# Optimization experiments

Hardware: AMD Instinct MI355X
Metric: run time of the kernel (lower is better)

The kernel has to match this reference:

```python
import jax, jax.numpy as jnp
import numpy as np

N_HEADS = 12
HEAD_DIM = 32
H_OUT = 28
W_OUT = 28
EPS_LN = 1e-6
EPS_TS = 1e-6


def _layer_norm(x, g, eps=EPS_LN):
    mu = jnp.mean(x, axis=-1, keepdims=True)
    xc = x - mu
    var = jnp.mean(xc * xc, axis=-1, keepdims=True)
    return xc * jax.lax.rsqrt(var + eps) * g


def setup_inputs() -> dict:
    key = jax.random.key(0)
    ks = jax.random.split(key, 6)
    b, hh, ww, d = 4, 56, 56, 384
    nc = 2 * H_OUT * W_OUT  # 1568
    s = 0.02
    return {
        "x": jax.random.normal(ks[0], (b, hh, ww, d), jnp.float32),
        "clusters": jax.random.normal(ks[1], (b, nc, d), jnp.float32),
        "g1": jnp.ones((d,), jnp.float32),
        "Wq": jax.random.normal(ks[2], (d, d), jnp.float32) * s,
        "Wkv": jax.random.normal(ks[3], (d, 2 * d), jnp.float32) * s,
        "Wo": jax.random.normal(ks[4], (d, d), jnp.float32) * s,
        "res_scale": jnp.ones((d,), jnp.float32),
        "g2": jnp.ones((2 * d,), jnp.float32),
        "Wproj": jax.random.normal(ks[5], (2 * d, 768), jnp.float32) * s,
    }


def reference(x, clusters, g1, Wq, Wkv, Wo, res_scale, g2, Wproj):
    b, hh, ww, d = x.shape
    n = hh * ww
    nc = clusters.shape[1]
    dh = HEAD_DIM
    scale = dh ** -0.5

    xf = x.reshape(b, n, d)
    xn = _layer_norm(xf, g1)
    cn = _layer_norm(clusters, g1)

    # projections; rearrange 'b n (h d) -> b h n d' and 'b n (k h d) -> k b h n d'
    q = (cn @ Wq).reshape(b, nc, N_HEADS, dh).transpose(0, 2, 1, 3)
    kv = (xn @ Wkv).reshape(b, n, 2, N_HEADS, dh)
    k = kv[:, :, 0].transpose(0, 2, 1, 3)  # [b h n dh]
    v = kv[:, :, 1].transpose(0, 2, 1, 3)

    attn = jnp.einsum('bhqd,bhkd->bhqk', q, k) * scale  # [b h nc n]
    # soft assignment: softmax over the query (cluster) axis
    attn = jax.nn.softmax(attn, axis=-2)
    token_sizes = attn.sum(-1)  # [b h nc]
    attn = attn / (token_sizes[..., None] + EPS_TS)
    token_sizes = token_sizes.mean(1)  # [b nc]

    c2 = jnp.einsum('bhqk,bhkd->bhqd', attn, v)
    c2 = c2.transpose(0, 2, 1, 3).reshape(b, nc, d) @ Wo

    token_sizes = token_sizes.reshape(b, nc // 2, 2).sum(-1)  # [b n']

    y = clusters * res_scale + c2
    y = y.reshape(b, nc // 2, 2 * d)  # 'b (n two) d -> b n (two d)'
    y = _layer_norm(y, g2) @ Wproj
    y = y.reshape(b, H_OUT, W_OUT, -1)
    token_sizes = token_sizes.reshape(b, H_OUT, W_OUT)
    return y, token_sizes
```

## Files before the change

kernel.cpp:

```cpp
#include <hip/hip_runtime.h>
#include <hip/hip_bf16.h>

typedef __hip_bfloat16 bf16;
typedef __attribute__((ext_vector_type(8))) short short8;
typedef __attribute__((ext_vector_type(4))) float f32x4;

#define B 4
#define NT 3136
#define NC 1568
#define NP 784
#define DMODEL 384
#define D2 768
#define NH 12
#define DH 32
#define KSPLIT 2
#define KSPLIT0 1600
#define SCALE 0.17677669529663687f
#define LOG2E 1.4426950408889634f
#define EPS_LN 1e-6f
#define EPS_TS 1e-6f

#if __has_builtin(__builtin_amdgcn_exp2f)
#define EXP2(x) __builtin_amdgcn_exp2f(x)
#else
#define EXP2(x) __expf(0.6931471805599453f * (x))
#endif

__device__ __forceinline__ unsigned short f2bf(float f) {
  return (unsigned short)(__bfloat16_as_ushort(__float2bfloat16(f)));
}
__device__ __forceinline__ float b2f(unsigned short u) {
  return __uint_as_float(((unsigned int)u) << 16);
}

__device__ __forceinline__ float lda(const void* __restrict__ p, size_t i,
                                     int mode, bool inf32) {
  bool f32 = (mode == 2) || (mode == 1 && inf32);
  return f32 ? ((const float*)p)[i]
             : __bfloat162float(((const bf16*)p)[i]);
}
__device__ __forceinline__ float4 lda4(const void* __restrict__ p, size_t i,
                                       int mode, bool inf32) {
  bool f32 = (mode == 2) || (mode == 1 && inf32);
  if (f32) return *(const float4*)((const float*)p + i);
  ushort4 u = *(const ushort4*)((const bf16*)p + i);
  return make_float4(b2f(u.x), b2f(u.y), b2f(u.z), b2f(u.w));
}

__global__ void sniff_kernel(const unsigned short* __restrict__ g1,
                             int* __restrict__ flag) {
  if (threadIdx.x == 0 && blockIdx.x == 0)
    *flag = (g1[0] == 0x3F80) ? 0 : 1;
}

__global__ void transpose_kernel(const void* __restrict__ in,
                                 const int* __restrict__ dtf,
                                 bf16* __restrict__ out, int K, int N,
                                 float scale) {
  bool inf32 = (*dtf != 0);
  __shared__ float t[32][33];
  int n0 = blockIdx.x * 32, k0 = blockIdx.y * 32;
  int tx = threadIdx.x & 31, ty = threadIdx.x >> 5;
#pragma unroll
  for (int s = 0; s < 32; s += 8)
    t[ty + s][tx] = lda(in, (size_t)(k0 + ty + s) * N + n0 + tx, 1, inf32);
  __syncthreads();
#pragma unroll
  for (int s = 0; s < 32; s += 8)
    out[(size_t)(n0 + ty + s) * K + k0 + tx] =
        __float2bfloat16(t[tx][ty + s] * scale);
}

__global__ void stats_kernel(const void* __restrict__ in, int mode,
                             const int* __restrict__ dtf,
                             float* __restrict__ stats, int D) {
  bool inf32 = (*dtf != 0);
  int row = blockIdx.x;
  int tid = threadIdx.x;
  size_t base = (size_t)row * D;
  int nper = D >> 7;
  float s = 0.f, s2 = 0.f;
  for (int i = 0; i < nper; i++) {
    float xv = lda(in, base + tid + (i << 7), mode, inf32);
    s += xv; s2 += xv * xv;
  }
  __shared__ float red[128], red2[128];
  red[tid] = s; red2[tid] = s2;
  __syncthreads();
  for (int off = 64; off > 0; off >>= 1) {
    if (tid < off) { red[tid] += red[tid + off]; red2[tid] += red2[tid + off]; }
    __syncthreads();
  }
  if (tid == 0) {
    float mean = red[0] / (float)D;
    float var  = red2[0] / (float)D - mean * mean;
    stats[row * 2]     = mean;
    stats[row * 2 + 1] = rsqrtf(var + EPS_LN);
  }
}

__global__ void __launch_bounds__(256, 3)
mgemm_kernel(const void* __restrict__ A, int a_mode, size_t a_bstr,
             const float* __restrict__ Astats, size_t s_bstr,
             const void* __restrict__ gammaA,
             const bf16* __restrict__ BT,
             const int* __restrict__ dtf,
             void* __restrict__ C, int c_f32, size_t c_bstr,
             bf16* __restrict__ Cv,
             int M, int N, int K,
             int epi,
             const void* __restrict__ resid, size_t r_bstr,
             const void* __restrict__ rscale) {
  bool inf32 = (*dtf != 0);
  int z = blockIdx.z;
  size_t a_off = (size_t)z * a_bstr;
  size_t r_off = (size_t)z * r_bstr;
  const float* st = Astats ? Astats + (size_t)z * s_bstr : nullptr;
  __shared__ __align__(16) unsigned short Asl[128][40];
  __shared__ __align__(16) unsigned short Bsl[128][40];
  int tid = threadIdx.x;
  int wave = tid >> 6, lane = tid & 63, l16 = lane & 15, quad = lane >> 4;
  int brow = blockIdx.y * 128, bcol = blockIdx.x * 128;
  int wm = (wave >> 1) * 64, wn = (wave & 1) * 64;
  f32x4 acc[4][4];
#pragma unroll
  for (int i = 0; i < 4; i++)
#pragma unroll
    for (int j = 0; j < 4; j++) acc[i][j] = (f32x4){0.f, 0.f, 0.f, 0.f};

  for (int k0 = 0; k0 < K; k0 += 32) {
#pragma unroll
    for (int it = 0; it < 4; it++) {
      int i = it * 256 + tid;
      int r = i >> 3, c4 = (i & 7) * 4;
      int grow = brow + r;
      if (grow >= M) grow = M - 1;
      float4 v = lda4(A, a_off + (size_t)grow * K + k0 + c4, a_mode, inf32);
      if (st) {
        float mu = st[grow * 2], rstd = st[grow * 2 + 1];
        float4 g = lda4(gammaA, k0 + c4, 1, inf32);
        v.x = (v.x - mu) * rstd * g.x; v.y = (v.y - mu) * rstd * g.y;
        v.z = (v.z - mu) * rstd * g.z; v.w = (v.w - mu) * rstd * g.w;
      }
      ushort4 u = {f2bf(v.x), f2bf(v.y), f2bf(v.z), f2bf(v.w)};
      *(ushort4*)&Asl[r][c4] = u;
    }
#pragma unroll
    for (int it = 0; it < 4; it++) {
      int i = it * 256 + tid;
      int r = i >> 3, c4 = (i & 7) * 4;
      *(ushort4*)&Bsl[r][c4] =
          *(const ushort4*)(BT + (size_t)(bcol + r) * K + k0 + c4);
    }
    __syncthreads();
    short8 af[4], bfr[4];
#pragma unroll
    for (int i = 0; i < 4; i++)
      af[i] = *(const short8*)&Asl[wm + 16 * i + l16][quad * 8];
#pragma unroll
    for (int j = 0; j < 4; j++)
      bfr[j] = *(const short8*)&Bsl[wn + 16 * j + l16][quad * 8];
#pragma unroll
    for (int i = 0; i < 4; i++)
#pragma unroll
      for (int j = 0; j < 4; j++)
        acc[i][j] = __builtin_amdgcn_mfma_f32_16x16x32_bf16(
            af[i], bfr[j], acc[i][j], 0, 0, 0);
    __syncthreads();
  }
#pragma unroll
  for (int i = 0; i < 4; i++) {
#pragma unroll
    for (int r = 0; r < 4; r++) {
      int m = brow + wm + 16 * i + quad * 4 + r;
      if (m < M) {
#pragma unroll
        for (int j = 0; j < 4; j++) {
          int n = bcol + wn + 16 * j + l16;
          float v = acc[i][j][r];
          if (epi == 1)
            v += lda(resid, r_off + (size_t)m * N + n, 1, inf32) *
                 lda(rscale, n, 1, inf32);
          if (epi == 2) {
            if (n < DMODEL) {
              ((bf16*)C)[(size_t)z * c_bstr + (size_t)m * DMODEL + n] =
                  __float2bfloat16(v);
            } else {
              int cc = n - DMODEL, hh = cc >> 5, dd = cc & 31;
              int w = m & 31;
              int pos = ((w >> 2) & 3) * 8 + (w >> 4) * 4 + (w & 3);
              Cv[(((size_t)z * NH + hh) * DH + dd) * NT + (m & ~31) + pos] =
                  __float2bfloat16(v);
            }
          } else {
            size_t idx = (size_t)z * c_bstr + (size_t)m * N + n;
            if (c_f32) ((float*)C)[idx] = v;
            else       ((bf16*)C)[idx]  = __float2bfloat16(v);
          }
        }
      }
    }
  }
}

__global__ void __launch_bounds__(256, 4)
sgemm_kernel(const void* __restrict__ A, int a_mode, size_t a_bstr,
             const float* __restrict__ Astats, size_t s_bstr,
             const void* __restrict__ gammaA,
             const bf16* __restrict__ BT,
             const int* __restrict__ dtf,
             void* __restrict__ C, int c_f32, size_t c_bstr,
             int M, int N, int K, int epi,
             const void* __restrict__ resid, size_t r_bstr,
             const void* __restrict__ rscale) {
  bool inf32 = (*dtf != 0);
  int z = blockIdx.z;
  size_t a_off = (size_t)z * a_bstr;
  size_t r_off = (size_t)z * r_bstr;
  const float* st = Astats ? Astats + (size_t)z * s_bstr : nullptr;
  int tid = threadIdx.x;
  int wave = tid >> 6, lane = tid & 63, l16 = lane & 15, quad = lane >> 4;
  int n0 = (blockIdx.x * 4 + wave) * 32;
  int m0 = blockIdx.y * 32;
  int ra = m0 + l16, rb = m0 + 16 + l16;
  int rca = (ra < M) ? ra : M - 1;
  int rcb = (rb < M) ? rb : M - 1;
  float mua = 0.f, rsa = 1.f, mub = 0.f, rsb = 1.f;
  if (st) {
    mua = st[rca * 2]; rsa = st[rca * 2 + 1];
    mub = st[rcb * 2]; rsb = st[rcb * 2 + 1];
  }
  const bf16* b0p = BT + (size_t)(n0 + l16) * K;
  const bf16* b1p = BT + (size_t)(n0 + 16 + l16) * K;
  f32x4 acc00 = {0.f, 0.f, 0.f, 0.f}, acc01 = {0.f, 0.f, 0.f, 0.f};
  f32x4 acc10 = {0.f, 0.f, 0.f, 0.f}, acc11 = {0.f, 0.f, 0.f, 0.f};
  for (int k0 = 0; k0 < K; k0 += 32) {
    int ka = k0 + quad * 8;
    float4 v0 = lda4(A, a_off + (size_t)rca * K + ka,     a_mode, inf32);
    float4 v1 = lda4(A, a_off + (size_t)rca * K + ka + 4, a_mode, inf32);
    float4 w0 = lda4(A, a_off + (size_t)rcb * K + ka,     a_mode, inf32);
    float4 w1 = lda4(A, a_off + (size_t)rcb * K + ka + 4, a_mode, inf32);
    if (st) {
      float4 g0  = lda4(gammaA, ka,     1, inf32);
      float4 g1v = lda4(gammaA, ka + 4, 1, inf32);
      v0.x = (v0.x - mua) * rsa * g0.x;  v0.y = (v0.y - mua) * rsa * g0.y;
      v0.z = (v0.z - mua) * rsa * g0.z;  v0.w = (v0.w - mua) * rsa * g0.w;
      v1.x = (v1.x - mua) * rsa * g1v.x; v1.y = (v1.y - mua) * rsa * g1v.y;
      v1.z = (v1.z - mua) * rsa * g1v.z; v1.w = (v1.w - mua) * rsa * g1v.w;
      w0.x = (w0.x - mub) * rsb * g0.x;  w0.y = (w0.y - mub) * rsb * g0.y;
      w0.z = (w0.z - mub) * rsb * g0.z;  w0.w = (w0.w - mub) * rsb * g0.w;
      w1.x = (w1.x - mub) * rsb * g1v.x; w1.y = (w1.y - mub) * rsb * g1v.y;
      w1.z = (w1.z - mub) * rsb * g1v.z; w1.w = (w1.w - mub) * rsb * g1v.w;
    }
    short8 afa, afb;
    afa[0] = (short)f2bf(v0.x); afa[1] = (short)f2bf(v0.y);
    afa[2] = (short)f2bf(v0.z); afa[3] = (short)f2bf(v0.w);
    afa[4] = (short)f2bf(v1.x); afa[5] = (short)f2bf(v1.y);
    afa[6] = (short)f2bf(v1.z); afa[7] = (short)f2bf(v1.w);
    afb[0] = (short)f2bf(w0.x); afb[1] = (short)f2bf(w0.y);
    afb[2] = (short)f2bf(w0.z); afb[3] = (short)f2bf(w0.w);
    afb[4] = (short)f2bf(w1.x); afb[5] = (short)f2bf(w1.y);
    afb[6] = (short)f2bf(w1.z); afb[7] = (short)f2bf(w1.w);
    short8 bf0 = *(const short8*)(b0p + ka);
    short8 bf1 = *(const short8*)(b1p + ka);
    acc00 = __builtin_amdgcn_mfma_f32_16x16x32_bf16(afa, bf0, acc00, 0, 0, 0);
    acc01 = __builtin_amdgcn_mfma_f32_16x16x32_bf16(afa, bf1, acc01, 0, 0, 0);
    acc10 = __builtin_amdgcn_mfma_f32_16x16x32_bf16(afb, bf0, acc10, 0, 0, 0);
    acc11 = __builtin_amdgcn_mfma_f32_16x16x32_bf16(afb, bf1, acc11, 0, 0, 0);
  }
#pragma unroll
  for (int i = 0; i < 2; i++) {
#pragma unroll
    for (int r = 0; r < 4; r++) {
      int m = m0 + 16 * i + quad * 4 + r;
      if (m >= M) continue;
      float v0 = (i == 0) ? acc00[r] : acc10[r];
      float v1 = (i == 0) ? acc01[r] : acc11[r];
      int nA = n0 + l16, nB = n0 + 16 + l16;
      if (epi == 1) {
        v0 += lda(resid, r_off + (size_t)m * N + nA, 1, inf32) *
              lda(rscale, nA, 1, inf32);
        v1 += lda(resid, r_off + (size_t)m * N + nB, 1, inf32) *
              lda(rscale, nB, 1, inf32);
      }
      size_t i0 = (size_t)z * c_bstr + (size_t)m * N + nA;
      size_t i1 = (size_t)z * c_bstr + (size_t)m * N + nB;
      if (c_f32) {
        ((float*)C)[i0] = v0;
        ((float*)C)[i1] = v1;
      } else {
        ((bf16*)C)[i0] = __float2bfloat16(v0);
        ((bf16*)C)[i1] = __float2bfloat16(v1);
      }
    }
  }
}

__global__ void __launch_bounds__(256, 4)
colsum_mfma(const bf16* __restrict__ qm, const bf16* __restrict__ km,
            float* __restrict__ l2ci) {
  int b = blockIdx.z, h = blockIdx.y;
  int tid = threadIdx.x;
  int wave = tid >> 6, lane = tid & 63, l16 = lane & 15, quad = lane >> 4;
  int key0 = blockIdx.x * 128 + wave * 32 + l16;
  int key1 = key0 + 16;
  int kc0 = (key0 < NT) ? key0 : NT - 1;
  int kc1 = (key1 < NT) ? key1 : NT - 1;
  short8 kf0 = *(const short8*)(km +
      ((size_t)(b * NT + kc0) * DMODEL + h * DH + quad * 8));
  short8 kf1 = *(const short8*)(km +
      ((size_t)(b * NT + kc1) * DMODEL + h * DH + quad * 8));
  __shared__ __align__(16) unsigned short Qlds[32][40];
  const bf16* qb = qm + (size_t)b * NC * DMODEL + h * DH;
  int srow = tid >> 3, sc4 = (tid & 7) * 4;
  float cs0 = 0.f, cs1 = 0.f;
  for (int q0 = 0; q0 < NC; q0 += 32) {
    ushort4 qu = *(const ushort4*)(qb + (size_t)(q0 + srow) * DMODEL + sc4);
    __syncthreads();
    *(ushort4*)&Qlds[srow][sc4] = qu;
    __syncthreads();
    short8 a1 = *(const short8*)&Qlds[l16][quad * 8];
    short8 a2 = *(const short8*)&Qlds[16 + l16][quad * 8];
    f32x4 z = {0.f, 0.f, 0.f, 0.f};
    f32x4 s10 = __builtin_amdgcn_mfma_f32_16x16x32_bf16(a1, kf0, z, 0, 0, 0);
    f32x4 s20 = __builtin_amdgcn_mfma_f32_16x16x32_bf16(a2, kf0, z, 0, 0, 0);
    f32x4 s11 = __builtin_amdgcn_mfma_f32_16x16x32_bf16(a1, kf1, z, 0, 0, 0);
    f32x4 s21 = __builtin_amdgcn_mfma_f32_16x16x32_bf16(a2, kf1, z, 0, 0, 0);
#pragma unroll
    for (int r = 0; r < 4; r++) {
      cs0 += EXP2(s10[r]) + EXP2(s20[r]);
      cs1 += EXP2(s11[r]) + EXP2(s21[r]);
    }
  }
  cs0 += __shfl_xor(cs0, 16, 64);
  cs0 += __shfl_xor(cs0, 32, 64);
  cs1 += __shfl_xor(cs1, 16, 64);
  cs1 += __shfl_xor(cs1, 32, 64);
  if (quad == 0) {
    if (key0 < NT) l2ci[((size_t)b * NH + h) * NT + key0] = -__log2f(cs0);
    if (key1 < NT) l2ci[((size_t)b * NH + h) * NT + key1] = -__log2f(cs1);
  }
}

__global__ void __launch_bounds__(256, 4)
pv_mfma(const bf16* __restrict__ qm, const bf16* __restrict__ km,
        const bf16* __restrict__ vt, const float* __restrict__ l2ci,
        float* __restrict__ po, float* __restrict__ prs) {
  int z = blockIdx.z;
  int b = z >> 1, split = z & 1;
  int h = blockIdx.y;
  int tid = threadIdx.x;
  int wave = tid >> 6, lane = tid & 63, l16 = lane & 15, quad = lane >> 4;
  int q0w = blockIdx.x * 128 + wave * 32;
  short8 qfrag[2];
#pragma unroll
  for (int t = 0; t < 2; t++) {
    int qr = q0w + t * 16 + l16; if (qr >= NC) qr = NC - 1;
    qfrag[t] = *(const short8*)(qm +
        ((size_t)(b * NC + qr) * DMODEL + h * DH + quad * 8));
  }
  __shared__ __align__(16) unsigned short Klds[64][40];
  __shared__ __align__(16) unsigned short Vlds[32][72];
  __shared__ __align__(16) float csl[64];
  f32x4 olo[2], ohi[2];
#pragma unroll
  for (int t = 0; t < 2; t++) {
    olo[t] = (f32x4){0.f, 0.f, 0.f, 0.f};
    ohi[t] = (f32x4){0.f, 0.f, 0.f, 0.f};
  }
  float rs[2] = {0.f, 0.f};
  const float* csb = l2ci + ((size_t)b * NH + h) * NT;
  const bf16* kb = km + (size_t)b * NT * DMODEL + h * DH;
  const bf16* vtb = vt + ((size_t)b * NH + h) * DH * NT;
  int krow = tid >> 2, kc8 = (tid & 3) * 8;
  int vrow = tid >> 3, vc8 = (tid & 7) * 8;
  int kbeg = split ? KSPLIT0 : 0;
  int kend = split ? NT : KSPLIT0;
  for (int k0 = kbeg; k0 < kend; k0 += 64) {
    short8 ku = *(const short8*)(kb + (size_t)(k0 + krow) * DMODEL + kc8);
    short8 vu = *(const short8*)(vtb + (size_t)vrow * NT + k0 + vc8);
    float4 cf;
    if (tid < 16) cf = *(const float4*)(csb + k0 + tid * 4);
    __syncthreads();
    *(short8*)&Klds[krow][kc8] = ku;
    *(short8*)&Vlds[vrow][vc8] = vu;
    if (tid < 16) *(float4*)&csl[tid * 4] = cf;
    __syncthreads();
#pragma unroll
    for (int ks = 0; ks < 64; ks += 32) {
      short8 kf1 = *(const short8*)&Klds[ks + l16][quad * 8];
      short8 kf2 = *(const short8*)&Klds[ks + 16 + l16][quad * 8];
      float4 ci1 = *(const float4*)&csl[ks + quad * 4];
      float4 ci2 = *(const float4*)&csl[ks + 16 + quad * 4];
      short8 vlo = *(const short8*)&Vlds[l16][ks + quad * 8];
      short8 vhi = *(const short8*)&Vlds[16 + l16][ks + quad * 8];
#pragma unroll
      for (int t = 0; t < 2; t++) {
        f32x4 z4 = {0.f, 0.f, 0.f, 0.f};
        f32x4 s1 = __builtin_amdgcn_mfma_f32_16x16x32_bf16(kf1, qfrag[t], z4, 0, 0, 0);
        f32x4 s2 = __builtin_amdgcn_mfma_f32_16x16x32_bf16(kf2, qfrag[t], z4, 0, 0, 0);
        float p0 = EXP2(s1[0] + ci1.x);
        float p1 = EXP2(s1[1] + ci1.y);
        float p2 = EXP2(s1[2] + ci1.z);
        float p3 = EXP2(s1[3] + ci1.w);
        float p4 = EXP2(s2[0] + ci2.x);
        float p5 = EXP2(s2[1] + ci2.y);
        float p6 = EXP2(s2[2] + ci2.z);
        float p7 = EXP2(s2[3] + ci2.w);
        rs[t] += ((p0 + p1) + (p2 + p3)) + ((p4 + p5) + (p6 + p7));
        short8 pf;
        pf[0] = (short)f2bf(p0); pf[1] = (short)f2bf(p1);
        pf[2] = (short)f2bf(p2); pf[3] = (short)f2bf(p3);
        pf[4] = (short)f2bf(p4); pf[5] = (short)f2bf(p5);
        pf[6] = (short)f2bf(p6); pf[7] = (short)f2bf(p7);
        olo[t] = __builtin_amdgcn_mfma_f32_16x16x32_bf16(pf, vlo, olo[t], 0, 0, 0);
        ohi[t] = __builtin_amdgcn_mfma_f32_16x16x32_bf16(pf, vhi, ohi[t], 0, 0, 0);
      }
    }
  }
#pragma unroll
  for (int t = 0; t < 2; t++) {
    rs[t] += __shfl_xor(rs[t], 16, 64);
    rs[t] += __shfl_xor(rs[t], 32, 64);
  }
  size_t pb = ((size_t)(split * B + b) * NH + h) * NC;
#pragma unroll
  for (int t = 0; t < 2; t++) {
#pragma unroll
    for (int r = 0; r < 4; r++) {
      int qloc = quad * 4 + r;
      int q = q0w + t * 16 + qloc;
      if (q < NC) {
        po[(pb + q) * 32 + l16]      = olo[t][r];
        po[(pb + q) * 32 + 16 + l16] = ohi[t][r];
      }
    }
    int qr = q0w + t * 16 + l16;
    if (quad == 0 && qr < NC) prs[pb + qr] = rs[t];
  }
}

__global__ void combine_kernel(const float* __restrict__ po,
                               const float* __restrict__ prs,
                               bf16* __restrict__ c2) {
  int bh = blockIdx.y;
  int tid = threadIdx.x;
  int q = blockIdx.x * 8 + (tid >> 5);
  int d = tid & 31;
  int b = bh / NH, h = bh - b * NH;
  size_t base0 = (size_t)bh * NC;
  size_t base1 = (size_t)B * NH * NC + base0;
  float o = po[(base0 + q) * 32 + d] + po[(base1 + q) * 32 + d];
  float rs = prs[base0 + q] + prs[base1 + q];
  c2[((size_t)b * NC + q) * DMODEL + h * 32 + d] =
      __float2bfloat16(o / (rs + EPS_TS));
}

__global__ void tok_kernel(const float* __restrict__ prs,
                           float* __restrict__ out_ts) {
  int idx = blockIdx.x * 256 + threadIdx.x;
  if (idx >= B * NP) return;
  int b = idx / NP, p = idx % NP;
  float s = 0.f;
  for (int h = 0; h < NH; h++) {
    size_t b0 = ((size_t)b * NH + h) * NC;
    size_t b1 = (size_t)B * NH * NC + b0;
    s += prs[b0 + 2 * p] + prs[b0 + 2 * p + 1] +
         prs[b1 + 2 * p] + prs[b1 + 2 * p + 1];
  }
  out_ts[idx] = s / (float)NH;
}

extern "C" void kernel_launch(void* const* d_in, const int* in_sizes, int n_in,
                              void* d_out, int out_size, void* d_ws, size_t ws_size,
                              hipStream_t stream) {
  const void* x         = d_in[0];
  const void* clusters  = d_in[1];
  const void* g1        = d_in[2];
  const void* Wq        = d_in[3];
  const void* Wkv       = d_in[4];
  const void* Wo        = d_in[5];
  const void* res_scale = d_in[6];
  const void* g2        = d_in[7];
  const void* Wproj     = d_in[8];
  float* out = (float*)d_out;

  float* fws = (float*)d_ws;
  size_t fo = 0;
  int*   dtf     = (int*)(fws + fo); fo += 4;
  float* stats_x = fws + fo; fo += (size_t)B * NT * 2;
  float* stats_c = fws + fo; fo += (size_t)B * NC * 2;
  float* stats_y = fws + fo; fo += (size_t)B * NP * 2;
  float* colsum  = fws + fo; fo += (size_t)B * NH * NT;
  float* prs     = fws + fo; fo += (size_t)KSPLIT * B * NH * NC;
  float* po      = fws + fo; fo += (size_t)KSPLIT * B * NC * DMODEL;
  float* y1f     = po;
  fo = (fo + 3) & ~(size_t)3;
  bf16* bws = (bf16*)(fws + fo);
  size_t o = 0;
  bf16* qm     = bws + o; o += (size_t)B * NC * DMODEL;
  bf16* km     = bws + o; o += (size_t)B * NT * DMODEL;
  bf16* vt     = bws + o; o += (size_t)B * NH * DH * NT;
  bf16* c2     = bws + o; o += (size_t)B * NC * DMODEL;
  bf16* wqT    = bws + o; o += (size_t)DMODEL * DMODEL;
  bf16* wkvT   = bws + o; o += (size_t)DMODEL * D2;
  bf16* woT    = bws + o; o += (size_t)DMODEL * DMODEL;
  bf16* wprojT = bws + o; o += (size_t)D2 * D2;

  const size_t xstr = (size_t)NT * DMODEL, cstr = (size_t)NC * DMODEL;
  const size_t ystr = (size_t)NP * D2;

  sniff_kernel<<<1, 1, 0, stream>>>((const unsigned short*)g1, dtf);
  transpose_kernel<<<dim3(DMODEL / 32, DMODEL / 32), 256, 0, stream>>>(
      Wq, dtf, wqT, DMODEL, DMODEL, SCALE * LOG2E);
  transpose_kernel<<<dim3(D2 / 32, DMODEL / 32), 256, 0, stream>>>(
      Wkv, dtf, wkvT, DMODEL, D2, 1.0f);
  transpose_kernel<<<dim3(DMODEL / 32, DMODEL / 32), 256, 0, stream>>>(
      Wo, dtf, woT, DMODEL, DMODEL, 1.0f);
  transpose_kernel<<<dim3(D2 / 32, D2 / 32), 256, 0, stream>>>(
      Wproj, dtf, wprojT, D2, D2, 1.0f);
  stats_kernel<<<B * NT, 128, 0, stream>>>(x, 1, dtf, stats_x, DMODEL);
  stats_kernel<<<B * NC, 128, 0, stream>>>(clusters, 1, dtf, stats_c, DMODEL);

  sgemm_kernel<<<dim3(DMODEL / 128, NC / 32, B), 256, 0, stream>>>(
      clusters, 1, cstr, stats_c, (size_t)NC * 2, g1, wqT, dtf,
      qm, 0, cstr, NC, DMODEL, DMODEL, 0, nullptr, 0, nullptr);
  mgemm_kernel<<<dim3(D2 / 128, (NT + 127) / 128, B), 256, 0, stream>>>(
      x, 1, xstr, stats_x, (size_t)NT * 2, g1, wkvT, dtf,
      km, 0, xstr, vt, NT, D2, DMODEL, 2, nullptr, 0, nullptr);
  colsum_mfma<<<dim3((NT + 127) / 128, NH, B), 256, 0, stream>>>(qm, km, colsum);
  pv_mfma<<<dim3((NC + 127) / 128, NH, B * KSPLIT), 256, 0, stream>>>(
      qm, km, vt, colsum, po, prs);
  combine_kernel<<<dim3(NC / 8, B * NH), 256, 0, stream>>>(po, prs, c2);
  sgemm_kernel<<<dim3(DMODEL / 128, NC / 32, B), 256, 0, stream>>>(
      c2, 0, cstr, nullptr, 0, nullptr, woT, dtf,
      y1f, 1, cstr, NC, DMODEL, DMODEL, 1, clusters, cstr, res_scale);
  stats_kernel<<<B * NP, 128, 0, stream>>>(y1f, 2, dtf, stats_y, D2);
  sgemm_kernel<<<dim3(D2 / 128, (NP + 31) / 32, B), 256, 0, stream>>>(
      y1f, 2, cstr, stats_y, (size_t)NP * 2, g2, wprojT, dtf,
      out, 1, ystr, NP, D2, D2, 0, nullptr, 0, nullptr);
  tok_kernel<<<(B * NP + 255) / 256, 256, 0, stream>>>(
      prs, out + (size_t)B * NP * D2);
}
```

Before: 384.5 us.

## Shrink GEMM row tiles to 16 and stage full-K normalized KV activations in LDS

```diff
diff --git a/kernel.cpp b/kernel.cpp
--- a/kernel.cpp
+++ b/kernel.cpp
@@ -99,147 +99,103 @@
   }
 }
 
-__global__ void __launch_bounds__(256, 3)
-mgemm_kernel(const void* __restrict__ A, int a_mode, size_t a_bstr,
-             const float* __restrict__ Astats, size_t s_bstr,
-             const void* __restrict__ gammaA,
-             const bf16* __restrict__ BT,
-             const int* __restrict__ dtf,
-             void* __restrict__ C, int c_f32, size_t c_bstr,
-             bf16* __restrict__ Cv,
-             int M, int N, int K,
-             int epi,
-             const void* __restrict__ resid, size_t r_bstr,
-             const void* __restrict__ rscale) {
+__global__ void __launch_bounds__(256, 4)
+kv_gemm(const void* __restrict__ A, size_t a_bstr,
+        const float* __restrict__ stats, size_t s_bstr,
+        const void* __restrict__ gamma,
+        const bf16* __restrict__ BT,
+        const int* __restrict__ dtf,
+        bf16* __restrict__ km, size_t c_bstr,
+        bf16* __restrict__ vt) {
+  bool inf32 = (*dtf != 0);
+  const int K = DMODEL;
+  int z = blockIdx.z;
+  size_t a_off = (size_t)z * a_bstr;
+  const float* st = stats + (size_t)z * s_bstr;
+  __shared__ __align__(16) unsigned short Asl[16][392];
+  int tid = threadIdx.x;
+  int wave = tid >> 6, lane = tid & 63, l16 = lane & 15, quad = lane >> 4;
+  int m0 = blockIdx.y * 16;
+  int n0 = (blockIdx.x * 4 + wave) * 32;
+  for (int it = 0; it < 6; it++) {
+    int i = it * 256 + tid;
+    int r = i / 96, c4 = (i - r * 96) * 4;
+    int grow = m0 + r;
+    float4 v = lda4(A, a_off + (size_t)grow * K + c4, 1, inf32);
+    float mu = st[grow * 2], rstd = st[grow * 2 + 1];
+    float4 g = lda4(gamma, c4, 1, inf32);
+    v.x = (v.x - mu) * rstd * g.x; v.y = (v.y - mu) * rstd * g.y;
+    v.z = (v.z - mu) * rstd * g.z; v.w = (v.w - mu) * rstd * g.w;
+    ushort4 u = {f2bf(v.x), f2bf(v.y), f2bf(v.z), f2bf(v.w)};
+    *(ushort4*)&Asl[r][c4] = u;
+  }
+  __syncthreads();
+  const bf16* b0p = BT + (size_t)(n0 + l16) * K;
+  const bf16* b1p = BT + (size_t)(n0 + 16 + l16) * K;
+  f32x4 acc00 = {0.f, 0.f, 0.f, 0.f}, acc01 = {0.f, 0.f, 0.f, 0.f};
+  for (int k0 = 0; k0 < K; k0 += 32) {
+    int ka = k0 + quad * 8;
+    short8 afa = *(const short8*)&Asl[l16][ka];
+    short8 bf0 = *(const short8*)(b0p + ka);
+    short8 bf1 = *(const short8*)(b1p + ka);
+    acc00 = __builtin_amdgcn_mfma_f32_16x16x32_bf16(afa, bf0, acc00, 0, 0, 0);
+    acc01 = __builtin_amdgcn_mfma_f32_16x16x32_bf16(afa, bf1, acc01, 0, 0, 0);
+  }
+#pragma unroll
+  for (int r = 0; r < 4; r++) {
+    int m = m0 + quad * 4 + r;
+    float v0 = acc00[r];
+    float v1 = acc01[r];
+    int nA = n0 + l16, nB = n0 + 16 + l16;
+    int w = m & 31;
+    int pos = ((w >> 2) & 3) * 8 + (w >> 4) * 4 + (w & 3);
+    if (nA < DMODEL) {
+      km[(size_t)z * c_bstr + (size_t)m * DMODEL + nA] = __float2bfloat16(v0);
+    } else {
+      int cc = nA - DMODEL, hh = cc >> 5, dd = cc & 31;
+      vt[(((size_t)z * NH + hh) * DH + dd) * NT + (m & ~31) + pos] =
+          __float2bfloat16(v0);
+    }
+    if (nB < DMODEL) {
+      km[(size_t)z * c_bstr + (size_t)m * DMODEL + nB] = __float2bfloat16(v1);
+    } else {
+      int cc = nB - DMODEL, hh = cc >> 5, dd = cc & 31;
+      vt[(((size_t)z * NH + hh) * DH + dd) * NT + (m & ~31) + pos] =
+          __float2bfloat16(v1);
+    }
+  }
+}
+
+__global__ void __launch_bounds__(256, 4)
+sgemm16_kernel(const void* __restrict__ A, int a_mode, size_t a_bstr,
+               const float* __restrict__ Astats, size_t s_bstr,
+               const void* __restrict__ gammaA,
+               const bf16* __restrict__ BT,
+               const int* __restrict__ dtf,
+               void* __restrict__ C, int c_f32, size_t c_bstr,
+               int M, int N, int K, int epi,
+               const void* __restrict__ resid, size_t r_bstr,
+               const void* __restrict__ rscale) {
   bool inf32 = (*dtf != 0);
   int z = blockIdx.z;
   size_t a_off = (size_t)z * a_bstr;
   size_t r_off = (size_t)z * r_bstr;
   const float* st = Astats ? Astats + (size_t)z * s_bstr : nullptr;
-  __shared__ __align__(16) unsigned short Asl[128][40];
-  __shared__ __align__(16) unsigned short Bsl[128][40];
-  int tid = threadIdx.x;
-  int wave = tid >> 6, lane = tid & 63, l16 = lane & 15, quad = lane >> 4;
-  int brow = blockIdx.y * 128, bcol = blockIdx.x * 128;
-  int wm = (wave >> 1) * 64, wn = (wave & 1) * 64;
-  f32x4 acc[4][4];
-#pragma unroll
-  for (int i = 0; i < 4; i++)
-#pragma unroll
-    for (int j = 0; j < 4; j++) acc[i][j] = (f32x4){0.f, 0.f, 0.f, 0.f};
-
-  for (int k0 = 0; k0 < K; k0 += 32) {
-#pragma unroll
-    for (int it = 0; it < 4; it++) {
-      int i = it * 256 + tid;
-      int r = i >> 3, c4 = (i & 7) * 4;
-      int grow = brow + r;
-      if (grow >= M) grow = M - 1;
-      float4 v = lda4(A, a_off + (size_t)grow * K + k0 + c4, a_mode, inf32);
-      if (st) {
-        float mu = st[grow * 2], rstd = st[grow * 2 + 1];
-        float4 g = lda4(gammaA, k0 + c4, 1, inf32);
-        v.x = (v.x - mu) * rstd * g.x; v.y = (v.y - mu) * rstd * g.y;
-        v.z = (v.z - mu) * rstd * g.z; v.w = (v.w - mu) * rstd * g.w;
-      }
-      ushort4 u = {f2bf(v.x), f2bf(v.y), f2bf(v.z), f2bf(v.w)};
-      *(ushort4*)&Asl[r][c4] = u;
-    }
-#pragma unroll
-    for (int it = 0; it < 4; it++) {
-      int i = it * 256 + tid;
-      int r = i >> 3, c4 = (i & 7) * 4;
-      *(ushort4*)&Bsl[r][c4] =
-          *(const ushort4*)(BT + (size_t)(bcol + r) * K + k0 + c4);
-    }
-    __syncthreads();
-    short8 af[4], bfr[4];
-#pragma unroll
-    for (int i = 0; i < 4; i++)
-      af[i] = *(const short8*)&Asl[wm + 16 * i + l16][quad * 8];
-#pragma unroll
-    for (int j = 0; j < 4; j++)
-      bfr[j] = *(const short8*)&Bsl[wn + 16 * j + l16][quad * 8];
-#pragma unroll
-    for (int i = 0; i < 4; i++)
-#pragma unroll
-      for (int j = 0; j < 4; j++)
-        acc[i][j] = __builtin_amdgcn_mfma_f32_16x16x32_bf16(
-            af[i], bfr[j], acc[i][j], 0, 0, 0);
-    __syncthreads();
-  }
-#pragma unroll
-  for (int i = 0; i < 4; i++) {
-#pragma unroll
-    for (int r = 0; r < 4; r++) {
-      int m = brow + wm + 16 * i + quad * 4 + r;
-      if (m < M) {
-#pragma unroll
-        for (int j = 0; j < 4; j++) {
-          int n = bcol + wn + 16 * j + l16;
-          float v = acc[i][j][r];
-          if (epi == 1)
-            v += lda(resid, r_off + (size_t)m * N + n, 1, inf32) *
-                 lda(rscale, n, 1, inf32);
-          if (epi == 2) {
-            if (n < DMODEL) {
-              ((bf16*)C)[(size_t)z * c_bstr + (size_t)m * DMODEL + n] =
-                  __float2bfloat16(v);
-            } else {
-              int cc = n - DMODEL, hh = cc >> 5, dd = cc & 31;
-              int w = m & 31;
-              int pos = ((w >> 2) & 3) * 8 + (w >> 4) * 4 + (w & 3);
-              Cv[(((size_t)z * NH + hh) * DH + dd) * NT + (m & ~31) + pos] =
-                  __float2bfloat16(v);
-            }
-          } else {
-            size_t idx = (size_t)z * c_bstr + (size_t)m * N + n;
-            if (c_f32) ((float*)C)[idx] = v;
-            else       ((bf16*)C)[idx]  = __float2bfloat16(v);
-          }
-        }
-      }
-    }
-  }
-}
-
-__global__ void __launch_bounds__(256, 4)
-sgemm_kernel(const void* __restrict__ A, int a_mode, size_t a_bstr,
-             const float* __restrict__ Astats, size_t s_bstr,
-             const void* __restrict__ gammaA,
-             const bf16* __restrict__ BT,
-             const int* __restrict__ dtf,
-             void* __restrict__ C, int c_f32, size_t c_bstr,
-             int M, int N, int K, int epi,
-             const void* __restrict__ resid, size_t r_bstr,
-             const void* __restrict__ rscale) {
-  bool inf32 = (*dtf != 0);
-  int z = blockIdx.z;
-  size_t a_off = (size_t)z * a_bstr;
-  size_t r_off = (size_t)z * r_bstr;
-  const float* st = Astats ? Astats + (size_t)z * s_bstr : nullptr;
   int tid = threadIdx.x;
   int wave = tid >> 6, lane = tid & 63, l16 = lane & 15, quad = lane >> 4;
   int n0 = (blockIdx.x * 4 + wave) * 32;
-  int m0 = blockIdx.y * 32;
-  int ra = m0 + l16, rb = m0 + 16 + l16;
+  int m0 = blockIdx.y * 16;
+  int ra = m0 + l16;
   int rca = (ra < M) ? ra : M - 1;
-  int rcb = (rb < M) ? rb : M - 1;
-  float mua = 0.f, rsa = 1.f, mub = 0.f, rsb = 1.f;
-  if (st) {
-    mua = st[rca * 2]; rsa = st[rca * 2 + 1];
-    mub = st[rcb * 2]; rsb = st[rcb * 2 + 1];
-  }
+  float mua = 0.f, rsa = 1.f;
+  if (st) { mua = st[rca * 2]; rsa = st[rca * 2 + 1]; }
   const bf16* b0p = BT + (size_t)(n0 + l16) * K;
   const bf16* b1p = BT + (size_t)(n0 + 16 + l16) * K;
   f32x4 acc00 = {0.f, 0.f, 0.f, 0.f}, acc01 = {0.f, 0.f, 0.f, 0.f};
-  f32x4 acc10 = {0.f, 0.f, 0.f, 0.f}, acc11 = {0.f, 0.f, 0.f, 0.f};
   for (int k0 = 0; k0 < K; k0 += 32) {
     int ka = k0 + quad * 8;
     float4 v0 = lda4(A, a_off + (size_t)rca * K + ka,     a_mode, inf32);
     float4 v1 = lda4(A, a_off + (size_t)rca * K + ka + 4, a_mode, inf32);
-    float4 w0 = lda4(A, a_off + (size_t)rcb * K + ka,     a_mode, inf32);
-    float4 w1 = lda4(A, a_off + (size_t)rcb * K + ka + 4, a_mode, inf32);
     if (st) {
       float4 g0  = lda4(gammaA, ka,     1, inf32);
       float4 g1v = lda4(gammaA, ka + 4, 1, inf32);
@@ -247,51 +203,38 @@
       v0.z = (v0.z - mua) * rsa * g0.z;  v0.w = (v0.w - mua) * rsa * g0.w;
       v1.x = (v1.x - mua) * rsa * g1v.x; v1.y = (v1.y - mua) * rsa * g1v.y;
       v1.z = (v1.z - mua) * rsa * g1v.z; v1.w = (v1.w - mua) * rsa * g1v.w;
-      w0.x = (w0.x - mub) * rsb * g0.x;  w0.y = (w0.y - mub) * rsb * g0.y;
-      w0.z = (w0.z - mub) * rsb * g0.z;  w0.w = (w0.w - mub) * rsb * g0.w;
-      w1.x = (w1.x - mub) * rsb * g1v.x; w1.y = (w1.y - mub) * rsb * g1v.y;
-      w1.z = (w1.z - mub) * rsb * g1v.z; w1.w = (w1.w - mub) * rsb * g1v.w;
-    }
-    short8 afa, afb;
+    }
+    short8 afa;
     afa[0] = (short)f2bf(v0.x); afa[1] = (short)f2bf(v0.y);
     afa[2] = (short)f2bf(v0.z); afa[3] = (short)f2bf(v0.w);
     afa[4] = (short)f2bf(v1.x); afa[5] = (short)f2bf(v1.y);
     afa[6] = (short)f2bf(v1.z); afa[7] = (short)f2bf(v1.w);
-    afb[0] = (short)f2bf(w0.x); afb[1] = (short)f2bf(w0.y);
-    afb[2] = (short)f2bf(w0.z); afb[3] = (short)f2bf(w0.w);
-    afb[4] = (short)f2bf(w1.x); afb[5] = (short)f2bf(w1.y);
-    afb[6] = (short)f2bf(w1.z); afb[7] = (short)f2bf(w1.w);
     short8 bf0 = *(const short8*)(b0p + ka);
     short8 bf1 = *(const short8*)(b1p + ka);
     acc00 = __builtin_amdgcn_mfma_f32_16x16x32_bf16(afa, bf0, acc00, 0, 0, 0);
     acc01 = __builtin_amdgcn_mfma_f32_16x16x32_bf16(afa, bf1, acc01, 0, 0, 0);
-    acc10 = __builtin_amdgcn_mfma_f32_16x16x32_bf16(afb, bf0, acc10, 0, 0, 0);
-    acc11 = __builtin_amdgcn_mfma_f32_16x16x32_bf16(afb, bf1, acc11, 0, 0, 0);
-  }
-#pragma unroll
-  for (int i = 0; i < 2; i++) {
-#pragma unroll
-    for (int r = 0; r < 4; r++) {
-      int m = m0 + 16 * i + quad * 4 + r;
-      if (m >= M) continue;
-      float v0 = (i == 0) ? acc00[r] : acc10[r];
-      float v1 = (i == 0) ? acc01[r] : acc11[r];
-      int nA = n0 + l16, nB = n0 + 16 + l16;
-      if (epi == 1) {
-        v0 += lda(resid, r_off + (size_t)m * N + nA, 1, inf32) *
-              lda(rscale, nA, 1, inf32);
-        v1 += lda(resid, r_off + (size_t)m * N + nB, 1, inf32) *
-              lda(rscale, nB, 1, inf32);
-      }
-      size_t i0 = (size_t)z * c_bstr + (size_t)m * N + nA;
-      size_t i1 = (size_t)z * c_bstr + (size_t)m * N + nB;
-      if (c_f32) {
-        ((float*)C)[i0] = v0;
-        ((float*)C)[i1] = v1;
-      } else {
-        ((bf16*)C)[i0] = __float2bfloat16(v0);
-        ((bf16*)C)[i1] = __float2bfloat16(v1);
-      }
+  }
+#pragma unroll
+  for (int r = 0; r < 4; r++) {
+    int m = m0 + quad * 4 + r;
+    if (m >= M) continue;
+    float v0 = acc00[r];
+    float v1 = acc01[r];
+    int nA = n0 + l16, nB = n0 + 16 + l16;
+    if (epi == 1) {
+      v0 += lda(resid, r_off + (size_t)m * N + nA, 1, inf32) *
+            lda(rscale, nA, 1, inf32);
+      v1 += lda(resid, r_off + (size_t)m * N + nB, 1, inf32) *
+            lda(rscale, nB, 1, inf32);
+    }
+    size_t i0 = (size_t)z * c_bstr + (size_t)m * N + nA;
+    size_t i1 = (size_t)z * c_bstr + (size_t)m * N + nB;
+    if (c_f32) {
+      ((float*)C)[i0] = v0;
+      ((float*)C)[i1] = v1;
+    } else {
+      ((bf16*)C)[i0] = __float2bfloat16(v0);
+      ((bf16*)C)[i1] = __float2bfloat16(v1);
     }
   }
 }
@@ -522,21 +465,20 @@
   stats_kernel<<<B * NT, 128, 0, stream>>>(x, 1, dtf, stats_x, DMODEL);
   stats_kernel<<<B * NC, 128, 0, stream>>>(clusters, 1, dtf, stats_c, DMODEL);
 
-  sgemm_kernel<<<dim3(DMODEL / 128, NC / 32, B), 256, 0, stream>>>(
+  sgemm16_kernel<<<dim3(DMODEL / 128, NC / 16, B), 256, 0, stream>>>(
       clusters, 1, cstr, stats_c, (size_t)NC * 2, g1, wqT, dtf,
       qm, 0, cstr, NC, DMODEL, DMODEL, 0, nullptr, 0, nullptr);
-  mgemm_kernel<<<dim3(D2 / 128, (NT + 127) / 128, B), 256, 0, stream>>>(
-      x, 1, xstr, stats_x, (size_t)NT * 2, g1, wkvT, dtf,
-      km, 0, xstr, vt, NT, D2, DMODEL, 2, nullptr, 0, nullptr);
+  kv_gemm<<<dim3(D2 / 128, NT / 16, B), 256, 0, stream>>>(
+      x, xstr, stats_x, (size_t)NT * 2, g1, wkvT, dtf, km, xstr, vt);
   colsum_mfma<<<dim3((NT + 127) / 128, NH, B), 256, 0, stream>>>(qm, km, colsum);
   pv_mfma<<<dim3((NC + 127) / 128, NH, B * KSPLIT), 256, 0, stream>>>(
       qm, km, vt, colsum, po, prs);
   combine_kernel<<<dim3(NC / 8, B * NH), 256, 0, stream>>>(po, prs, c2);
-  sgemm_kernel<<<dim3(DMODEL / 128, NC / 32, B), 256, 0, stream>>>(
+  sgemm16_kernel<<<dim3(DMODEL / 128, NC / 16, B), 256, 0, stream>>>(
       c2, 0, cstr, nullptr, 0, nullptr, woT, dtf,
       y1f, 1, cstr, NC, DMODEL, DMODEL, 1, clusters, cstr, res_scale);
   stats_kernel<<<B * NP, 128, 0, stream>>>(y1f, 2, dtf, stats_y, D2);
-  sgemm_kernel<<<dim3(D2 / 128, (NP + 31) / 32, B), 256, 0, stream>>>(
+  sgemm16_kernel<<<dim3(D2 / 128, NP / 16, B), 256, 0, stream>>>(
       y1f, 2, cstr, stats_y, (size_t)NP * 2, g2, wprojT, dtf,
       out, 1, ystr, NP, D2, D2, 0, nullptr, 0, nullptr);
   tok_kernel<<<(B * NP + 255) / 256, 256, 0, stream>>>(
```

After: 427.1 us. 1.11x slower.
